# Kernel optimization log

Measured on AMD Instinct MI355X. Metric: run time of the kernel, lower is better.

Reference implementation:

```python
import jax, jax.numpy as jnp
import numpy as np

NSAMPLE = 64
RADIUS = 0.3
HMIN = -0.2
HMAX_LIST = (0.1, 0.2, 0.3, 0.4)
NUM_ANGLE = 12
NUM_DEPTH = 4
EPS = 1e-5


def setup_inputs() -> dict:
    key = jax.random.key(0)
    ks = jax.random.split(key, 32)
    rn = lambda i, s: jax.random.normal(ks[i], s, dtype=jnp.float32)
    ru = lambda i, s: jax.random.uniform(ks[i], s, dtype=jnp.float32)
    return {
        'seed_xyz': rn(0, (2, 1024, 3)),
        'pointcloud': rn(1, (2, 8192, 3)),
        'vp_rot': rn(2, (2, 1024, 3, 3)),
        'cw1': rn(3, (64, 3)), 'cbn1': ru(4, (4, 64)),
        'cw2': rn(5, (128, 64)), 'cbn2': ru(6, (4, 128)),
        'cw3': rn(7, (256, 128)), 'cbn3': ru(8, (4, 256)),
        'ow1': rn(9, (128, 256)), 'ob1': rn(10, (128,)), 'obn1': ru(11, (4, 128)),
        'ow2': rn(12, (128, 128)), 'ob2': rn(13, (128,)), 'obn2': ru(14, (4, 128)),
        'ow3': rn(15, (36, 128)), 'ob3': rn(16, (36,)),
        'tw1': rn(17, (128, 256)), 'tb1': rn(18, (128,)), 'tbn1': ru(19, (4, 128)),
        'tw2': rn(20, (128, 128)), 'tb2': rn(21, (128,)), 'tbn2': ru(22, (4, 128)),
        'tw3': rn(23, (12, 128)), 'tb3': rn(24, (12,)),
    }


def _bn_relu(y, bn):
    g, b, m, v = bn[0], bn[1], bn[2], bn[3]
    return jax.nn.relu(g * (y - m) * jax.lax.rsqrt(v + EPS) + b)


def _bn(y, bn):
    g, b, m, v = bn[0], bn[1], bn[2], bn[3]
    return g * (y - m) * jax.lax.rsqrt(v + EPS) + b


def _forward(seed_xyz, pointcloud, vp_rot, cw1, cbn1, cw2, cbn2, cw3, cbn3,
             ow1, ob1, obn1, ow2, ob2, obn2, ow3, ob3,
             tw1, tb1, tbn1, tw2, tb2, tbn2, tw3, tb3):
    B, ns, _ = seed_xyz.shape
    N = pointcloud.shape[1]
    # relative coords of every scene point w.r.t. every seed, rotated into the
    # grasp-view frame (cylinder axis = x after rotation): (B, ns, N, 3)
    rel = pointcloud[:, None, :, :] - seed_xyz[:, :, None, :]
    rot_rel = jnp.einsum('bsnc,bscd->bsnd', rel, vp_rot)
    ax = rot_rel[..., 0]
    r2 = rot_rel[..., 1] ** 2 + rot_rel[..., 2] ** 2
    pref = jnp.arange(N, dtype=jnp.float32) / N  # earlier index preferred (CUDA scan order)
    groups = []
    for hmax in HMAX_LIST:
        mask = (ax > HMIN) & (ax < hmax) & (r2 < RADIUS * RADIUS)
        score = mask.astype(jnp.float32) * 2.0 - pref
        _, idx = jax.lax.top_k(score, NSAMPLE)  # (B, ns, NSAMPLE), first valid idxs in order
        valid = jnp.take_along_axis(mask, idx, axis=-1)
        idx = jnp.where(valid, idx, idx[..., :1])  # fill slots with first found index
        g = jnp.take_along_axis(rot_rel, idx[..., None], axis=2)  # (B, ns, NSAMPLE, 3)
        groups.append(g)
    feat = jnp.stack(groups, axis=2)  # (B, ns, num_depth, NSAMPLE, 3)
    feat = feat.reshape(B, ns * NUM_DEPTH, NSAMPLE, 3)
    # SharedMLP [3,64,128,256], conv2d 1x1 (no bias) + BN + ReLU
    h = _bn_relu(feat @ cw1.T, cbn1)
    h = _bn_relu(h @ cw2.T, cbn2)
    h = _bn_relu(h @ cw3.T, cbn3)
    vp = jnp.max(h, axis=2)  # max-pool over nsample -> (B, ns*num_depth, 256)

    def head(w1, b1, bn1, w2, b2, bn2, w3, b3):
        x = _bn_relu(vp @ w1.T + b1, bn1)
        x = _bn_relu(x @ w2.T + b2, bn2)
        return x @ w3.T + b3

    op = head(ow1, ob1, obn1, ow2, ob2, obn2, ow3, ob3)     # (B, ns*D, 3*num_angle)
    tol = head(tw1, tb1, tbn1, tw2, tb2, tbn2, tw3, tb3)    # (B, ns*D, num_angle)
    out = jnp.concatenate([op, tol], axis=-1)               # score|angle_cls|width|tolerance
    out = out.reshape(B, ns, NUM_DEPTH, 4 * NUM_ANGLE).transpose(0, 3, 1, 2)
    return out  # (B, 4*num_angle, num_seed, num_depth)


def reference(seed_xyz, pointcloud, vp_rot, cw1, cbn1, cw2, cbn2, cw3, cbn3,
              ow1, ob1, obn1, ow2, ob2, obn2, ow3, ob3,
              tw1, tb1, tbn1, tw2, tb2, tbn2, tw3, tb3):
    return _forward(seed_xyz, pointcloud, vp_rot, cw1, cbn1, cw2, cbn2, cw3, cbn3,
                    ow1, ob1, obn1, ow2, ob2, obn2, ow3, ob3,
                    tw1, tb1, tbn1, tw2, tb2, tbn2, tw3, tb3)
```

## Files before the change

kernel.cpp:

```cpp
#include <hip/hip_runtime.h>
#include <hip/hip_bf16.h>

#define NB    2
#define NS    1024
#define NPTS  8192
#define NGROUP (NB*NS*4)

enum : int {
  OFF_BW2  = 256,
  OFF_W1Q  = 4352,
  OFF_B2   = 8448,
  OFF_BW3  = 8576,
  OFF_B3   = 41344,
  OFF_HB1  = 41600,
  OFF_HB1B = 74368,
  OFF_HB2  = 74624,
  OFF_HB2B = 107392,
  OFF_HB3  = 107648,
  OFF_HB3B = 115840,
  OFF_FEAT = 146688,
  OFF_VP   = 1719552,
  OFF_PCX  = 1719552, OFF_PCY = 1735936, OFF_PCZ = 1752320,
  OFF_SEED = 1768704, OFF_ROT = 1774848,
  OFF_CNT  = 3816704,
  OFF_FLAG = 3824896,
  PREP_TOTAL = 189632 + 6144 + 18432 + 49152,
};

struct Ptrs { const void* p[25]; };

typedef __attribute__((ext_vector_type(8))) short bf16x8;
typedef __attribute__((ext_vector_type(4))) float f32x4;
typedef __attribute__((ext_vector_type(4))) unsigned u32x4;

template<typename T> struct LD;
template<> struct LD<float> {
  static __device__ __forceinline__ float get(const void* p, int i){ return ((const float*)p)[i]; }
};
template<> struct LD<__hip_bfloat16> {
  static __device__ __forceinline__ float get(const void* p, int i){ return __bfloat162float(((const __hip_bfloat16*)p)[i]); }
};

template<typename T>
__device__ __forceinline__ float bnscale(const void* bn, int C, int c){
  float g = LD<T>::get(bn, c);
  float v = LD<T>::get(bn, 3*C + c);
  return g / sqrtf(v + 1e-5f);
}

__device__ __forceinline__ unsigned short f2bf(float v){
  __hip_bfloat16 hb = __float2bfloat16(v);
  return *reinterpret_cast<unsigned short*>(&hb);
}

#if __has_builtin(__builtin_amdgcn_cvt_pk_bf16_f32)
typedef __attribute__((ext_vector_type(2))) __bf16 bf16x2_t;
__device__ __forceinline__ unsigned pk2bf(float a, float b){
  bf16x2_t r = __builtin_amdgcn_cvt_pk_bf16_f32(a, b);
  return *reinterpret_cast<unsigned*>(&r);
}
#else
__device__ __forceinline__ unsigned pk2bf(float a, float b){
  return (unsigned)f2bf(a) | ((unsigned)f2bf(b) << 16);
}
#endif

template<typename T>
__device__ void prep_body(const Ptrs& in, float* __restrict__ ws, int i){
  if (i < 256) { int c = i>>2, d = i&3; float s = bnscale<T>(in.p[4],64,c);
    float v = (d<3) ? LD<T>::get(in.p[3], c*3+d)*s
                    : LD<T>::get(in.p[4],64+c) - LD<T>::get(in.p[4],2*64+c)*s;
    ws[OFF_W1Q+i] = v; return; }
  i -= 256;
  if (i < 8192) {
    int j = i&7, f = i>>3, lane = f&63, kn = f>>6, kt = kn&1, nt = kn>>1;
    int n = nt*16 + (lane&15), k = kt*32 + ((lane>>4)<<3) + j;
    float s = bnscale<T>(in.p[6],128,n);
    ((unsigned short*)(ws + OFF_BW2))[i] = f2bf(LD<T>::get(in.p[5], n*64+k)*s); return; }
  i -= 8192;
  if (i < 32768) {
    int j = i&7, f = i>>3, lane = f&63, kn = f>>6, kt = kn&3, nt = kn>>2;
    int n = nt*16 + (lane&15), k = kt*32 + ((lane>>4)<<3) + j;
    float s = bnscale<T>(in.p[8],256,n);
    ((unsigned short*)(ws + OFF_BW3))[i] = f2bf(LD<T>::get(in.p[7], n*128+k)*s); return; }
  i -= 32768;
  if (i < 128) { float s = bnscale<T>(in.p[6],128,i);
    ws[OFF_B2+i] = LD<T>::get(in.p[6],128+i) - LD<T>::get(in.p[6],2*128+i)*s; return; }
  i -= 128;
  if (i < 256) { float s = bnscale<T>(in.p[8],256,i);
    ws[OFF_B3+i] = LD<T>::get(in.p[8],256+i) - LD<T>::get(in.p[8],2*256+i)*s; return; }
  i -= 256;
  if (i < 65536) {
    int j = i&7, f = i>>3, lane = f&63, kn = f>>6, kt = kn&7, nt = kn>>3;
    int n = nt*16 + (lane&15), k = kt*32 + ((lane>>4)<<3) + j;
    float v;
    if (n < 128) v = LD<T>::get(in.p[9],  n*256+k)       * bnscale<T>(in.p[11],128,n);
    else         v = LD<T>::get(in.p[17], (n-128)*256+k) * bnscale<T>(in.p[19],128,n-128);
    ((unsigned short*)(ws + OFF_HB1))[i] = f2bf(v); return; }
  i -= 65536;
  if (i < 256) { int n = i; float v;
    if (n < 128) { float s = bnscale<T>(in.p[11],128,n);
      v = (LD<T>::get(in.p[10],n) - LD<T>::get(in.p[11],2*128+n))*s + LD<T>::get(in.p[11],128+n); }
    else { int m = n-128; float s = bnscale<T>(in.p[19],128,m);
      v = (LD<T>::get(in.p[18],m) - LD<T>::get(in.p[19],2*128+m))*s + LD<T>::get(in.p[19],128+m); }
    ws[OFF_HB1B+n] = v; return; }
  i -= 256;
  if (i < 65536) {
    int j = i&7, f = i>>3, lane = f&63, kn = f>>6, kt = kn&7, nt = kn>>3;
    int n = nt*16 + (lane&15), k = kt*32 + ((lane>>4)<<3) + j;
    float v = 0.f;
    if (n < 128) { if (k < 128)  v = LD<T>::get(in.p[12], n*128+k)            * bnscale<T>(in.p[14],128,n); }
    else         { if (k >= 128) v = LD<T>::get(in.p[20], (n-128)*128+(k-128)) * bnscale<T>(in.p[22],128,n-128); }
    ((unsigned short*)(ws + OFF_HB2))[i] = f2bf(v); return; }
  i -= 65536;
  if (i < 256) { int n = i; float v;
    if (n < 128) { float s = bnscale<T>(in.p[14],128,n);
      v = (LD<T>::get(in.p[13],n) - LD<T>::get(in.p[14],2*128+n))*s + LD<T>::get(in.p[14],128+n); }
    else { int m = n-128; float s = bnscale<T>(in.p[22],128,m);
      v = (LD<T>::get(in.p[21],m) - LD<T>::get(in.p[22],2*128+m))*s + LD<T>::get(in.p[22],128+m); }
    ws[OFF_HB2B+n] = v; return; }
  i -= 256;
  if (i < 16384) {
    int j = i&7, f = i>>3, lane = f&63, kn = f>>6, kt = kn&7, nt = kn>>3;
    int n = nt*16 + (lane&15), k = kt*32 + ((lane>>4)<<3) + j;
    float v = 0.f;
    if (n < 36)      { if (k < 128)  v = LD<T>::get(in.p[15], n*128+k); }
    else if (n < 48) { if (k >= 128) v = LD<T>::get(in.p[23], (n-36)*128+(k-128)); }
    ((unsigned short*)(ws + OFF_HB3))[i] = f2bf(v); return; }
  i -= 16384;
  if (i < 64) { int n = i; float v = 0.f;
    if (n < 36) v = LD<T>::get(in.p[16], n);
    else if (n < 48) v = LD<T>::get(in.p[24], n-36);
    ws[OFF_HB3B+n] = v; return; }
  i -= 64;
  if (i < 6144)  { ws[OFF_SEED+i] = LD<T>::get(in.p[0], i); return; }
  i -= 6144;
  if (i < 18432) { ws[OFF_ROT+i] = LD<T>::get(in.p[2], i); return; }
  i -= 18432;
  { int arr = i >> 14, idx = i & 16383;
    ws[OFF_PCX + arr*16384 + idx] = LD<T>::get(in.p[1], idx*3 + arr); }
}

__global__ __launch_bounds__(256) void prep_kernel(Ptrs in, float* __restrict__ ws){
  __shared__ int sf;
  const int t = threadIdx.x;
  if (t == 0) sf = 0;
  __syncthreads();
  int loc = 0;
  const uint4* w3r = (const uint4*)in.p[7];
#pragma unroll
  for (int k = 0; k < 2; ++k) {
    uint4 u = w3r[t + k*256];
    loc |= ((u.x & 0x7F80u) == 0x7F80u) | (((u.x>>16) & 0x7F80u) == 0x7F80u);
    loc |= ((u.y & 0x7F80u) == 0x7F80u) | (((u.y>>16) & 0x7F80u) == 0x7F80u);
    loc |= ((u.z & 0x7F80u) == 0x7F80u) | (((u.z>>16) & 0x7F80u) == 0x7F80u);
    loc |= ((u.w & 0x7F80u) == 0x7F80u) | (((u.w>>16) & 0x7F80u) == 0x7F80u);
  }
  if (loc) atomicOr(&sf, 1);
  __syncthreads();
  const int isf32 = sf;
  const int i = blockIdx.x*256 + t;
  if (i == 0) ((int*)(ws + OFF_FLAG))[0] = isf32;
  if (i >= PREP_TOTAL) return;
  if (isf32) prep_body<float>(in, ws, i);
  else       prep_body<__hip_bfloat16>(in, ws, i);
}

__global__ __launch_bounds__(256) void group_kernel(float* __restrict__ ws){
#pragma clang fp contract(off)
  __shared__ float scratch[2][2][4][192];
  __shared__ int   cl[2][2][4];
  __shared__ float p0s[2][3];
  const int t = threadIdx.x;
  const int wave = t >> 6, lane = t & 63;
  const int s = wave >> 1, half = wave & 1;
  const int seedIdx = blockIdx.x*2 + s;
  const int b = seedIdx >> 10;
  const float sx = ws[OFF_SEED + seedIdx*3+0];
  const float sy = ws[OFF_SEED + seedIdx*3+1];
  const float sz = ws[OFF_SEED + seedIdx*3+2];
  const float r00=ws[OFF_ROT+seedIdx*9+0], r01=ws[OFF_ROT+seedIdx*9+1], r02=ws[OFF_ROT+seedIdx*9+2];
  const float r10=ws[OFF_ROT+seedIdx*9+3], r11=ws[OFF_ROT+seedIdx*9+4], r12=ws[OFF_ROT+seedIdx*9+5];
  const float r20=ws[OFF_ROT+seedIdx*9+6], r21=ws[OFF_ROT+seedIdx*9+7], r22=ws[OFF_ROT+seedIdx*9+8];
  const float* px = ws + OFF_PCX + b*8192;
  const float* py = ws + OFF_PCY + b*8192;
  const float* pz = ws + OFF_PCZ + b*8192;
  if (half == 0 && lane == 0) {
    float e0 = px[0] - sx, e1 = py[0] - sy, e2 = pz[0] - sz;
    p0s[s][0] = e0*r00 + e1*r10 + e2*r20;
    p0s[s][1] = e0*r01 + e1*r11 + e2*r21;
    p0s[s][2] = e0*r02 + e1*r12 + e2*r22;
  }
  float* s0 = scratch[s][half][0];
  float* s1 = scratch[s][half][1];
  float* s2 = scratch[s][half][2];
  float* s3 = scratch[s][half][3];
  int c0n=0, c1n=0, c2n=0, c3n=0;
  const int basept = half*4096;
  const unsigned long long pm = (1ull << lane) - 1ull;

  auto scan = [&](float x, float y, float z){
    float e0 = x - sx, e1 = y - sy, e2 = z - sz;
    float rx = e0*r00 + e1*r10 + e2*r20;
    float ry = e0*r01 + e1*r11 + e2*r21;
    float rz = e0*r02 + e1*r12 + e2*r22;
    float r2 = ry*ry + rz*rz;
    const bool mb = (rx > -0.2f) && (r2 < 0.09f);
    const bool l3 = mb && (rx < 0.4f);
    const unsigned long long bal3 = __ballot(l3);
    if (bal3 == 0ull) return;
    { bool m = mb && (rx < 0.1f); unsigned long long bal = __ballot(m);
      if (bal) { int slot = c0n + __popcll(bal & pm);
        if (m && slot < 64) { s0[slot*3]=rx; s0[slot*3+1]=ry; s0[slot*3+2]=rz; }
        c0n += __popcll(bal); } }
    { bool m = mb && (rx < 0.2f); unsigned long long bal = __ballot(m);
      if (bal) { int slot = c1n + __popcll(bal & pm);
        if (m && slot < 64) { s1[slot*3]=rx; s1[slot*3+1]=ry; s1[slot*3+2]=rz; }
        c1n += __popcll(bal); } }
    { bool m = mb && (rx < 0.3f); unsigned long long bal = __ballot(m);
      if (bal) { int slot = c2n + __popcll(bal & pm);
        if (m && slot < 64) { s2[slot*3]=rx; s2[slot*3+1]=ry; s2[slot*3+2]=rz; }
        c2n += __popcll(bal); } }
    { int slot = c3n + __popcll(bal3 & pm);
      if (l3 && slot < 64) { s3[slot*3]=rx; s3[slot*3+1]=ry; s3[slot*3+2]=rz; }
      c3n += __popcll(bal3); }
  };

  for (int c = 0; c < 64; c += 2) {
    const int i0 = basept + c*64 + lane;
    float xA = px[i0],    yA = py[i0],    zA = pz[i0];
    float xB = px[i0+64], yB = py[i0+64], zB = pz[i0+64];
    scan(xA, yA, zA);
    scan(xB, yB, zB);
  }
  if (lane == 0) { cl[s][half][0]=c0n; cl[s][half][1]=c1n; cl[s][half][2]=c2n; cl[s][half][3]=c3n; }
  __syncthreads();
  for (int idx = t; idx < 512; idx += 256) {
    const int ss = idx >> 8, bin = (idx >> 6) & 3, slot = idx & 63;
    int ca = cl[ss][0][bin]; if (ca > 64) ca = 64;
    int cb = cl[ss][1][bin];
    const float* A = scratch[ss][0][bin];
    const float* B = scratch[ss][1][bin];
    float fx, fy, fz;
    if (slot < ca)              { fx=A[slot*3]; fy=A[slot*3+1]; fz=A[slot*3+2]; }
    else if (slot - ca < cb)    { int q = slot-ca; fx=B[q*3]; fy=B[q*3+1]; fz=B[q*3+2]; }
    else if (ca > 0)            { fx=A[0]; fy=A[1]; fz=A[2]; }
    else if (cb > 0)            { fx=B[0]; fy=B[1]; fz=B[2]; }
    else                        { fx=p0s[ss][0]; fy=p0s[ss][1]; fz=p0s[ss][2]; }
    const int g = (blockIdx.x*2 + ss)*4 + bin;
    float* fo = ws + OFF_FEAT + g*192;
    fo[slot*3+0]=fx; fo[slot*3+1]=fy; fo[slot*3+2]=fz;
  }
  if (t < 8) {
    const int ss = t >> 2, bin = t & 3;
    int tot = cl[ss][0][bin] + cl[ss][1][bin];
    if (tot > 64) tot = 64;
    if (tot < 1)  tot = 1;
    const int g = (blockIdx.x*2 + ss)*4 + bin;
    ((int*)(ws + OFF_CNT))[g] = (tot + 15) >> 4;
  }
}

template<int MTS>
__device__ __forceinline__ void mlp_body(float* __restrict__ ws, unsigned short* __restrict__ h2,
                                         const float* __restrict__ wq,
                                         int lane, int quad, int l15, int nhalf, int g){
  const float* feat = ws + OFF_FEAT + g*192;
  float fx[MTS], fy[MTS], fz[MTS];
#pragma unroll
  for (int Nt = 0; Nt < MTS; ++Nt) {
    const int sm = Nt*16 + l15;
    fx[Nt] = feat[sm*3+0]; fy[Nt] = feat[sm*3+1]; fz[Nt] = feat[sm*3+2];
  }
  bf16x8 b1[MTS][2];
#pragma unroll
  for (int kt = 0; kt < 2; ++kt) {
    f32x4 w[8];
#pragma unroll
    for (int j = 0; j < 8; ++j) w[j] = *(const f32x4*)(wq + (kt*32 + quad*8 + j)*4);
#pragma unroll
    for (int Nt = 0; Nt < MTS; ++Nt) {
      const float x0 = fx[Nt], x1 = fy[Nt], x2 = fz[Nt];
      u32x4 p;
#pragma unroll
      for (int jp = 0; jp < 4; ++jp) {
        const f32x4 wa = w[2*jp], wb = w[2*jp+1];
        const float v0 = fmaxf(wa[3] + x0*wa[0] + x1*wa[1] + x2*wa[2], 0.f);
        const float v1 = fmaxf(wb[3] + x0*wb[0] + x1*wb[1] + x2*wb[2], 0.f);
        p[jp] = pk2bf(v0, v1);
      }
      b1[Nt][kt] = __builtin_bit_cast(bf16x8, p);
    }
  }
  const bf16x8* BW2 = (const bf16x8*)(ws + OFF_BW2);
#pragma unroll
  for (int mt4 = 0; mt4 < 4; ++mt4) {
    const int Mt = nhalf*4 + mt4;
    const f32x4 bias4 = *(const f32x4*)(ws + OFF_B2 + Mt*16 + quad*4);
    f32x4 acc[MTS];
#pragma unroll
    for (int Nt = 0; Nt < MTS; ++Nt) acc[Nt] = bias4;
#pragma unroll
    for (int kt = 0; kt < 2; ++kt) {
      const bf16x8 aw = BW2[(Mt*2+kt)*64 + lane];
#pragma unroll
      for (int Nt = 0; Nt < MTS; ++Nt)
        acc[Nt] = __builtin_amdgcn_mfma_f32_16x16x32_bf16(aw, b1[Nt][kt], acc[Nt], 0, 0, 0);
    }
#pragma unroll
    for (int Nt = 0; Nt < MTS; ++Nt) {
      const unsigned lo = pk2bf(fmaxf(acc[Nt][0],0.f), fmaxf(acc[Nt][1],0.f));
      const unsigned hi = pk2bf(fmaxf(acc[Nt][2],0.f), fmaxf(acc[Nt][3],0.f));
      uint2* dst = (uint2*)&h2[(Nt*16 + l15)*136 + Mt*16 + quad*4];
      *dst = make_uint2(lo, hi);
    }
  }
  __syncthreads();
  bf16x8 a2[MTS][4];
#pragma unroll
  for (int mt = 0; mt < MTS; ++mt)
#pragma unroll
    for (int kt = 0; kt < 4; ++kt)
      a2[mt][kt] = *(const bf16x8*)&h2[(mt*16 + l15)*136 + kt*32 + quad*8];
  const bf16x8* BW3 = (const bf16x8*)(ws + OFF_BW3);
  float vpv[8];
#pragma unroll
  for (int nt8 = 0; nt8 < 8; ++nt8) {
    const int nt = nhalf*8 + nt8;
    const int n = nt*16 + l15;
    const float bias = ws[OFF_B3 + n];
    f32x4 acc[MTS];
#pragma unroll
    for (int mt = 0; mt < MTS; ++mt) acc[mt] = (f32x4){bias, bias, bias, bias};
#pragma unroll
    for (int kt = 0; kt < 4; ++kt) {
      const bf16x8 b = BW3[(nt*4+kt)*64 + lane];
#pragma unroll
      for (int mt = 0; mt < MTS; ++mt)
        acc[mt] = __builtin_amdgcn_mfma_f32_16x16x32_bf16(a2[mt][kt], b, acc[mt], 0, 0, 0);
    }
    float mx = 0.f;
#pragma unroll
    for (int mt = 0; mt < MTS; ++mt)
      mx = fmaxf(mx, fmaxf(fmaxf(acc[mt][0], acc[mt][1]), fmaxf(acc[mt][2], acc[mt][3])));
    mx = fmaxf(mx, __shfl_xor(mx, 16, 64));
    mx = fmaxf(mx, __shfl_xor(mx, 32, 64));
    vpv[nt8] = mx;
  }
  if (quad == 0) {
    float* vp = ws + OFF_VP + g*256 + nhalf*128;
#pragma unroll
    for (int nt8 = 0; nt8 < 8; ++nt8) vp[nt8*16 + l15] = vpv[nt8];
  }
}

__global__ __launch_bounds__(256) void mlp_kernel(float* __restrict__ ws){
  __shared__ unsigned short h2s[2][64*136];
  const int blk = blockIdx.x;
  const int g0 = blk*2, g1 = blk*2 + 1;
  const int* cnt = (const int*)(ws + OFF_CNT);
  const int mt0 = cnt[g0], mt1 = cnt[g1];
  const int v = (mt0 > mt1) ? mt0 : mt1;
  const int t = threadIdx.x;
  const int wave = t >> 6, lane = t & 63;
  const int quad = lane >> 4, l15 = lane & 15;
  const int grp = wave >> 1, nhalf = wave & 1;
  const int g = grp ? g1 : g0;
  unsigned short* h2 = h2s[grp];
  const float* wq = ws + OFF_W1Q;
  switch (v) {
    case 1:  mlp_body<1>(ws, h2, wq, lane, quad, l15, nhalf, g); break;
    case 2:  mlp_body<2>(ws, h2, wq, lane, quad, l15, nhalf, g); break;
    case 3:  mlp_body<3>(ws, h2, wq, lane, quad, l15, nhalf, g); break;
    default: mlp_body<4>(ws, h2, wq, lane, quad, l15, nhalf, g); break;
  }
}

#define YSTRIDE 264
__global__ __launch_bounds__(256) void heads_kernel(float* __restrict__ ws, void* __restrict__ outv){
  const int isf32 = ((const volatile int*)(ws + OFF_FLAG))[0];
  __shared__ unsigned short y[16*YSTRIDE];
  const int t = threadIdx.x;
  const int wave = t >> 6, lane = t & 63;
  const int quad = lane >> 4, l15 = lane & 15;
  const int r0 = blockIdx.x * 16;
  bf16x8 a[8];
  const float* vp = ws + OFF_VP + (r0 + l15)*256;
#pragma unroll
  for (int kt = 0; kt < 8; ++kt) {
    const float4* v4 = (const float4*)(vp + kt*32 + quad*8);
    float4 u0 = v4[0], u1 = v4[1];
    a[kt][0]=(short)f2bf(u0.x); a[kt][1]=(short)f2bf(u0.y); a[kt][2]=(short)f2bf(u0.z); a[kt][3]=(short)f2bf(u0.w);
    a[kt][4]=(short)f2bf(u1.x); a[kt][5]=(short)f2bf(u1.y); a[kt][6]=(short)f2bf(u1.z); a[kt][7]=(short)f2bf(u1.w);
  }
  const bf16x8* HB1 = (const bf16x8*)(ws + OFF_HB1);
#pragma unroll
  for (int nt4 = 0; nt4 < 4; ++nt4) {
    const int nt = wave*4 + nt4;
    const int n = nt*16 + l15;
    const float bias = ws[OFF_HB1B + n];
    f32x4 acc = (f32x4){bias, bias, bias, bias};
#pragma unroll
    for (int kt = 0; kt < 8; ++kt)
      acc = __builtin_amdgcn_mfma_f32_16x16x32_bf16(a[kt], HB1[(nt*8+kt)*64 + lane], acc, 0, 0, 0);
#pragma unroll
    for (int jj = 0; jj < 4; ++jj)
      y[(quad*4+jj)*YSTRIDE + n] = f2bf(fmaxf(acc[jj], 0.f));
  }
  __syncthreads();
#pragma unroll
  for (int kt = 0; kt < 8; ++kt)
    a[kt] = *(const bf16x8*)&y[l15*YSTRIDE + kt*32 + quad*8];
  __syncthreads();
  const bf16x8* HB2 = (const bf16x8*)(ws + OFF_HB2);
#pragma unroll
  for (int nt4 = 0; nt4 < 4; ++nt4) {
    const int nt = wave*4 + nt4;
    const int n = nt*16 + l15;
    const float bias = ws[OFF_HB2B + n];
    f32x4 acc = (f32x4){bias, bias, bias, bias};
#pragma unroll
    for (int kt = 0; kt < 8; ++kt)
      acc = __builtin_amdgcn_mfma_f32_16x16x32_bf16(a[kt], HB2[(nt*8+kt)*64 + lane], acc, 0, 0, 0);
#pragma unroll
    for (int jj = 0; jj < 4; ++jj)
      y[(quad*4+jj)*YSTRIDE + n] = f2bf(fmaxf(acc[jj], 0.f));
  }
  __syncthreads();
#pragma unroll
  for (int kt = 0; kt < 8; ++kt)
    a[kt] = *(const bf16x8*)&y[l15*YSTRIDE + kt*32 + quad*8];
  const bf16x8* HB3 = (const bf16x8*)(ws + OFF_HB3);
  {
    const int n = wave*16 + l15;
    const float bias = ws[OFF_HB3B + n];
    f32x4 acc = (f32x4){bias, bias, bias, bias};
#pragma unroll
    for (int kt = 0; kt < 8; ++kt)
      acc = __builtin_amdgcn_mfma_f32_16x16x32_bf16(a[kt], HB3[(wave*8+kt)*64 + lane], acc, 0, 0, 0);
    if (n < 48) {
#pragma unroll
      for (int jj = 0; jj < 4; ++jj) {
        const int gr = r0 + quad*4 + jj;
        const int b = gr >> 12, rem = gr & 4095, s = rem >> 2, d = rem & 3;
        const int o = ((b*48 + n)*1024 + s)*4 + d;
        if (isf32) ((float*)outv)[o] = acc[jj];
        else       ((__hip_bfloat16*)outv)[o] = __float2bfloat16(acc[jj]);
      }
    }
  }
}

extern "C" void kernel_launch(void* const* d_in, const int* in_sizes, int n_in,
                              void* d_out, int out_size, void* d_ws, size_t ws_size,
                              hipStream_t stream) {
  float* ws = (float*)d_ws;
  Ptrs P;
  for (int i = 0; i < 25; ++i) P.p[i] = d_in[i];
  prep_kernel<<<(PREP_TOTAL+255)/256, 256, 0, stream>>>(P, ws);
  group_kernel<<<NB*NS/2, 256, 0, stream>>>(ws);
  mlp_kernel<<<NGROUP/2, 256, 0, stream>>>(ws);
  heads_kernel<<<NGROUP/16, 256, 0, stream>>>(ws, d_out);
}
```

Measured before the change: 206.3 us.

## Fuse grouping, shared MLP and heads into one kernel using LDS intermediates

Result: no change. 208.0 us (+0.8%).

```diff
diff --git a/kernel.cpp b/kernel.cpp
--- a/kernel.cpp
+++ b/kernel.cpp
@@ -18,11 +18,8 @@
   OFF_HB2B = 107392,
   OFF_HB3  = 107648,
   OFF_HB3B = 115840,
-  OFF_FEAT = 146688,
-  OFF_VP   = 1719552,
   OFF_PCX  = 1719552, OFF_PCY = 1735936, OFF_PCZ = 1752320,
   OFF_SEED = 1768704, OFF_ROT = 1774848,
-  OFF_CNT  = 3816704,
   OFF_FLAG = 3824896,
   PREP_TOTAL = 189632 + 6144 + 18432 + 49152,
 };
@@ -166,15 +163,14 @@
   else       prep_body<__hip_bfloat16>(in, ws, i);
 }
 
-__global__ __launch_bounds__(256) void group_kernel(float* __restrict__ ws){
+__device__ void group_phase(const float* __restrict__ ws, float* __restrict__ scratch,
+                            int* __restrict__ cl, float* __restrict__ p0s,
+                            float* __restrict__ featL, int* __restrict__ mtL,
+                            int blk, int t){
 #pragma clang fp contract(off)
-  __shared__ float scratch[2][2][4][192];
-  __shared__ int   cl[2][2][4];
-  __shared__ float p0s[2][3];
-  const int t = threadIdx.x;
   const int wave = t >> 6, lane = t & 63;
   const int s = wave >> 1, half = wave & 1;
-  const int seedIdx = blockIdx.x*2 + s;
+  const int seedIdx = blk*2 + s;
   const int b = seedIdx >> 10;
   const float sx = ws[OFF_SEED + seedIdx*3+0];
   const float sy = ws[OFF_SEED + seedIdx*3+1];
@@ -187,14 +183,14 @@
   const float* pz = ws + OFF_PCZ + b*8192;
   if (half == 0 && lane == 0) {
     float e0 = px[0] - sx, e1 = py[0] - sy, e2 = pz[0] - sz;
-    p0s[s][0] = e0*r00 + e1*r10 + e2*r20;
-    p0s[s][1] = e0*r01 + e1*r11 + e2*r21;
-    p0s[s][2] = e0*r02 + e1*r12 + e2*r22;
-  }
-  float* s0 = scratch[s][half][0];
-  float* s1 = scratch[s][half][1];
-  float* s2 = scratch[s][half][2];
-  float* s3 = scratch[s][half][3];
+    p0s[s*3+0] = e0*r00 + e1*r10 + e2*r20;
+    p0s[s*3+1] = e0*r01 + e1*r11 + e2*r21;
+    p0s[s*3+2] = e0*r02 + e1*r12 + e2*r22;
+  }
+  float* s0 = scratch + ((s*2+half)*4+0)*192;
+  float* s1 = scratch + ((s*2+half)*4+1)*192;
+  float* s2 = scratch + ((s*2+half)*4+2)*192;
+  float* s3 = scratch + ((s*2+half)*4+3)*192;
   int c0n=0, c1n=0, c2n=0, c3n=0;
   const int basept = half*4096;
   const unsigned long long pm = (1ull << lane) - 1ull;
@@ -233,44 +229,45 @@
     scan(xA, yA, zA);
     scan(xB, yB, zB);
   }
-  if (lane == 0) { cl[s][half][0]=c0n; cl[s][half][1]=c1n; cl[s][half][2]=c2n; cl[s][half][3]=c3n; }
+  if (lane == 0) {
+    cl[(s*2+half)*4+0]=c0n; cl[(s*2+half)*4+1]=c1n;
+    cl[(s*2+half)*4+2]=c2n; cl[(s*2+half)*4+3]=c3n;
+  }
   __syncthreads();
   for (int idx = t; idx < 512; idx += 256) {
     const int ss = idx >> 8, bin = (idx >> 6) & 3, slot = idx & 63;
-    int ca = cl[ss][0][bin]; if (ca > 64) ca = 64;
-    int cb = cl[ss][1][bin];
-    const float* A = scratch[ss][0][bin];
-    const float* B = scratch[ss][1][bin];
+    int ca = cl[(ss*2+0)*4+bin]; if (ca > 64) ca = 64;
+    int cb = cl[(ss*2+1)*4+bin];
+    const float* A = scratch + ((ss*2+0)*4+bin)*192;
+    const float* B = scratch + ((ss*2+1)*4+bin)*192;
     float fx, fy, fz;
     if (slot < ca)              { fx=A[slot*3]; fy=A[slot*3+1]; fz=A[slot*3+2]; }
     else if (slot - ca < cb)    { int q = slot-ca; fx=B[q*3]; fy=B[q*3+1]; fz=B[q*3+2]; }
     else if (ca > 0)            { fx=A[0]; fy=A[1]; fz=A[2]; }
     else if (cb > 0)            { fx=B[0]; fy=B[1]; fz=B[2]; }
-    else                        { fx=p0s[ss][0]; fy=p0s[ss][1]; fz=p0s[ss][2]; }
-    const int g = (blockIdx.x*2 + ss)*4 + bin;
-    float* fo = ws + OFF_FEAT + g*192;
+    else                        { fx=p0s[ss*3+0]; fy=p0s[ss*3+1]; fz=p0s[ss*3+2]; }
+    float* fo = featL + (ss*4+bin)*192;
     fo[slot*3+0]=fx; fo[slot*3+1]=fy; fo[slot*3+2]=fz;
   }
   if (t < 8) {
     const int ss = t >> 2, bin = t & 3;
-    int tot = cl[ss][0][bin] + cl[ss][1][bin];
+    int tot = cl[(ss*2+0)*4+bin] + cl[(ss*2+1)*4+bin];
     if (tot > 64) tot = 64;
     if (tot < 1)  tot = 1;
-    const int g = (blockIdx.x*2 + ss)*4 + bin;
-    ((int*)(ws + OFF_CNT))[g] = (tot + 15) >> 4;
+    mtL[t] = (tot + 15) >> 4;
   }
 }
 
 template<int MTS>
-__device__ __forceinline__ void mlp_body(float* __restrict__ ws, unsigned short* __restrict__ h2,
-                                         const float* __restrict__ wq,
-                                         int lane, int quad, int l15, int nhalf, int g){
-  const float* feat = ws + OFF_FEAT + g*192;
+__device__ __forceinline__ void mlp_body(const float* __restrict__ ws, unsigned short* __restrict__ h2,
+                                         const float* __restrict__ wq, const float* __restrict__ featp,
+                                         float* __restrict__ vpp,
+                                         int lane, int quad, int l15, int nhalf){
   float fx[MTS], fy[MTS], fz[MTS];
 #pragma unroll
   for (int Nt = 0; Nt < MTS; ++Nt) {
     const int sm = Nt*16 + l15;
-    fx[Nt] = feat[sm*3+0]; fy[Nt] = feat[sm*3+1]; fz[Nt] = feat[sm*3+2];
+    fx[Nt] = featp[sm*3+0]; fy[Nt] = featp[sm*3+1]; fz[Nt] = featp[sm*3+2];
   }
   bf16x8 b1[MTS][2];
 #pragma unroll
@@ -348,104 +345,120 @@
     vpv[nt8] = mx;
   }
   if (quad == 0) {
-    float* vp = ws + OFF_VP + g*256 + nhalf*128;
-#pragma unroll
-    for (int nt8 = 0; nt8 < 8; ++nt8) vp[nt8*16 + l15] = vpv[nt8];
-  }
-}
-
-__global__ __launch_bounds__(256) void mlp_kernel(float* __restrict__ ws){
-  __shared__ unsigned short h2s[2][64*136];
-  const int blk = blockIdx.x;
-  const int g0 = blk*2, g1 = blk*2 + 1;
-  const int* cnt = (const int*)(ws + OFF_CNT);
-  const int mt0 = cnt[g0], mt1 = cnt[g1];
-  const int v = (mt0 > mt1) ? mt0 : mt1;
+#pragma unroll
+    for (int nt8 = 0; nt8 < 8; ++nt8) vpp[nhalf*128 + nt8*16 + l15] = vpv[nt8];
+  }
+}
+
+#define YSTRIDE 264
+__global__ __launch_bounds__(256) void fused_kernel(float* __restrict__ ws, void* __restrict__ outv){
+  __shared__ __align__(16) char ubuf[34816];
+  __shared__ float featL[8*192];
+  __shared__ float vpL[8*256];
+  __shared__ int   mtL[8];
+  __shared__ float w1qL[1024];
   const int t = threadIdx.x;
   const int wave = t >> 6, lane = t & 63;
   const int quad = lane >> 4, l15 = lane & 15;
-  const int grp = wave >> 1, nhalf = wave & 1;
-  const int g = grp ? g1 : g0;
-  unsigned short* h2 = h2s[grp];
-  const float* wq = ws + OFF_W1Q;
-  switch (v) {
-    case 1:  mlp_body<1>(ws, h2, wq, lane, quad, l15, nhalf, g); break;
-    case 2:  mlp_body<2>(ws, h2, wq, lane, quad, l15, nhalf, g); break;
-    case 3:  mlp_body<3>(ws, h2, wq, lane, quad, l15, nhalf, g); break;
-    default: mlp_body<4>(ws, h2, wq, lane, quad, l15, nhalf, g); break;
-  }
-}
-
-#define YSTRIDE 264
-__global__ __launch_bounds__(256) void heads_kernel(float* __restrict__ ws, void* __restrict__ outv){
-  const int isf32 = ((const volatile int*)(ws + OFF_FLAG))[0];
-  __shared__ unsigned short y[16*YSTRIDE];
-  const int t = threadIdx.x;
-  const int wave = t >> 6, lane = t & 63;
-  const int quad = lane >> 4, l15 = lane & 15;
-  const int r0 = blockIdx.x * 16;
-  bf16x8 a[8];
-  const float* vp = ws + OFF_VP + (r0 + l15)*256;
-#pragma unroll
-  for (int kt = 0; kt < 8; ++kt) {
-    const float4* v4 = (const float4*)(vp + kt*32 + quad*8);
-    float4 u0 = v4[0], u1 = v4[1];
-    a[kt][0]=(short)f2bf(u0.x); a[kt][1]=(short)f2bf(u0.y); a[kt][2]=(short)f2bf(u0.z); a[kt][3]=(short)f2bf(u0.w);
-    a[kt][4]=(short)f2bf(u1.x); a[kt][5]=(short)f2bf(u1.y); a[kt][6]=(short)f2bf(u1.z); a[kt][7]=(short)f2bf(u1.w);
-  }
-  const bf16x8* HB1 = (const bf16x8*)(ws + OFF_HB1);
-#pragma unroll
-  for (int nt4 = 0; nt4 < 4; ++nt4) {
-    const int nt = wave*4 + nt4;
-    const int n = nt*16 + l15;
-    const float bias = ws[OFF_HB1B + n];
-    f32x4 acc = (f32x4){bias, bias, bias, bias};
+  const int blk = blockIdx.x;
+
+  for (int i = t; i < 1024; i += 256) w1qL[i] = ws[OFF_W1Q + i];
+
+  group_phase(ws, (float*)ubuf, (int*)(ubuf + 12288), (float*)(ubuf + 12288 + 64),
+              featL, mtL, blk, t);
+  __syncthreads();
+
+  {
+    const int grp = wave >> 1, nhalf = wave & 1;
+    unsigned short* h2 = (unsigned short*)ubuf + grp*(64*136);
+    for (int pair = 0; pair < 4; ++pair) {
+      const int m0 = mtL[pair*2], m1 = mtL[pair*2+1];
+      const int v = (m0 > m1) ? m0 : m1;
+      const int lg = pair*2 + grp;
+      const float* featp = featL + lg*192;
+      float* vpp = vpL + lg*256;
+      switch (v) {
+        case 1:  mlp_body<1>(ws, h2, w1qL, featp, vpp, lane, quad, l15, nhalf); break;
+        case 2:  mlp_body<2>(ws, h2, w1qL, featp, vpp, lane, quad, l15, nhalf); break;
+        case 3:  mlp_body<3>(ws, h2, w1qL, featp, vpp, lane, quad, l15, nhalf); break;
+        default: mlp_body<4>(ws, h2, w1qL, featp, vpp, lane, quad, l15, nhalf); break;
+      }
+      __syncthreads();
+    }
+  }
+
+  {
+    const int isf32 = ((const volatile int*)(ws + OFF_FLAG))[0];
+    unsigned short* y = (unsigned short*)ubuf;
+    bf16x8 a[8];
+    if (l15 < 8) {
+      const float* vp = vpL + l15*256;
+#pragma unroll
+      for (int kt = 0; kt < 8; ++kt) {
+        const float4* v4 = (const float4*)(vp + kt*32 + quad*8);
+        float4 u0 = v4[0], u1 = v4[1];
+        a[kt][0]=(short)f2bf(u0.x); a[kt][1]=(short)f2bf(u0.y); a[kt][2]=(short)f2bf(u0.z); a[kt][3]=(short)f2bf(u0.w);
+        a[kt][4]=(short)f2bf(u1.x); a[kt][5]=(short)f2bf(u1.y); a[kt][6]=(short)f2bf(u1.z); a[kt][7]=(short)f2bf(u1.w);
+      }
+    } else {
+      const u32x4 z = (u32x4){0,0,0,0};
+#pragma unroll
+      for (int kt = 0; kt < 8; ++kt) a[kt] = __builtin_bit_cast(bf16x8, z);
+    }
+    const bf16x8* HB1 = (const bf16x8*)(ws + OFF_HB1);
+#pragma unroll
+    for (int nt4 = 0; nt4 < 4; ++nt4) {
+      const int nt = wave*4 + nt4;
+      const int n = nt*16 + l15;
+      const float bias = ws[OFF_HB1B + n];
+      f32x4 acc = (f32x4){bias, bias, bias, bias};
+#pragma unroll
+      for (int kt = 0; kt < 8; ++kt)
+        acc = __builtin_amdgcn_mfma_f32_16x16x32_bf16(a[kt], HB1[(nt*8+kt)*64 + lane], acc, 0, 0, 0);
+#pragma unroll
+      for (int jj = 0; jj < 4; ++jj)
+        y[(quad*4+jj)*YSTRIDE + n] = f2bf(fmaxf(acc[jj], 0.f));
+    }
+    __syncthreads();
 #pragma unroll
     for (int kt = 0; kt < 8; ++kt)
-      acc = __builtin_amdgcn_mfma_f32_16x16x32_bf16(a[kt], HB1[(nt*8+kt)*64 + lane], acc, 0, 0, 0);
-#pragma unroll
-    for (int jj = 0; jj < 4; ++jj)
-      y[(quad*4+jj)*YSTRIDE + n] = f2bf(fmaxf(acc[jj], 0.f));
-  }
-  __syncthreads();
-#pragma unroll
-  for (int kt = 0; kt < 8; ++kt)
-    a[kt] = *(const bf16x8*)&y[l15*YSTRIDE + kt*32 + quad*8];
-  __syncthreads();
-  const bf16x8* HB2 = (const bf16x8*)(ws + OFF_HB2);
-#pragma unroll
-  for (int nt4 = 0; nt4 < 4; ++nt4) {
-    const int nt = wave*4 + nt4;
-    const int n = nt*16 + l15;
-    const float bias = ws[OFF_HB2B + n];
-    f32x4 acc = (f32x4){bias, bias, bias, bias};
+      a[kt] = *(const bf16x8*)&y[l15*YSTRIDE + kt*32 + quad*8];
+    __syncthreads();
+    const bf16x8* HB2 = (const bf16x8*)(ws + OFF_HB2);
+#pragma unroll
+    for (int nt4 = 0; nt4 < 4; ++nt4) {
+      const int nt = wave*4 + nt4;
+      const int n = nt*16 + l15;
+      const float bias = ws[OFF_HB2B + n];
+      f32x4 acc = (f32x4){bias, bias, bias, bias};
+#pragma unroll
+      for (int kt = 0; kt < 8; ++kt)
+        acc = __builtin_amdgcn_mfma_f32_16x16x32_bf16(a[kt], HB2[(nt*8+kt)*64 + lane], acc, 0, 0, 0);
+#pragma unroll
+      for (int jj = 0; jj < 4; ++jj)
+        y[(quad*4+jj)*YSTRIDE + n] = f2bf(fmaxf(acc[jj], 0.f));
+    }
+    __syncthreads();
 #pragma unroll
     for (int kt = 0; kt < 8; ++kt)
-      acc = __builtin_amdgcn_mfma_f32_16x16x32_bf16(a[kt], HB2[(nt*8+kt)*64 + lane], acc, 0, 0, 0);
-#pragma unroll
-    for (int jj = 0; jj < 4; ++jj)
-      y[(quad*4+jj)*YSTRIDE + n] = f2bf(fmaxf(acc[jj], 0.f));
-  }
-  __syncthreads();
-#pragma unroll
-  for (int kt = 0; kt < 8; ++kt)
-    a[kt] = *(const bf16x8*)&y[l15*YSTRIDE + kt*32 + quad*8];
-  const bf16x8* HB3 = (const bf16x8*)(ws + OFF_HB3);
-  {
-    const int n = wave*16 + l15;
-    const float bias = ws[OFF_HB3B + n];
-    f32x4 acc = (f32x4){bias, bias, bias, bias};
-#pragma unroll
-    for (int kt = 0; kt < 8; ++kt)
-      acc = __builtin_amdgcn_mfma_f32_16x16x32_bf16(a[kt], HB3[(wave*8+kt)*64 + lane], acc, 0, 0, 0);
-    if (n < 48) {
-#pragma unroll
-      for (int jj = 0; jj < 4; ++jj) {
-        const int gr = r0 + quad*4 + jj;
-        const int b = gr >> 12, rem = gr & 4095, s = rem >> 2, d = rem & 3;
-        const int o = ((b*48 + n)*1024 + s)*4 + d;
-        if (isf32) ((float*)outv)[o] = acc[jj];
-        else       ((__hip_bfloat16*)outv)[o] = __float2bfloat16(acc[jj]);
+      a[kt] = *(const bf16x8*)&y[l15*YSTRIDE + kt*32 + quad*8];
+    const bf16x8* HB3 = (const bf16x8*)(ws + OFF_HB3);
+    {
+      const int n = wave*16 + l15;
+      const float bias = ws[OFF_HB3B + n];
+      f32x4 acc = (f32x4){bias, bias, bias, bias};
+#pragma unroll
+      for (int kt = 0; kt < 8; ++kt)
+        acc = __builtin_amdgcn_mfma_f32_16x16x32_bf16(a[kt], HB3[(wave*8+kt)*64 + lane], acc, 0, 0, 0);
+      if (n < 48 && quad < 2) {
+#pragma unroll
+        for (int jj = 0; jj < 4; ++jj) {
+          const int gr = blk*8 + quad*4 + jj;
+          const int b = gr >> 12, rem = gr & 4095, s = rem >> 2, d = rem & 3;
+          const int o = ((b*48 + n)*1024 + s)*4 + d;
+          if (isf32) ((float*)outv)[o] = acc[jj];
+          else       ((__hip_bfloat16*)outv)[o] = __float2bfloat16(acc[jj]);
+        }
       }
     }
   }
@@ -458,7 +471,5 @@
   Ptrs P;
   for (int i = 0; i < 25; ++i) P.p[i] = d_in[i];
   prep_kernel<<<(PREP_TOTAL+255)/256, 256, 0, stream>>>(P, ws);
-  group_kernel<<<NB*NS/2, 256, 0, stream>>>(ws);
-  mlp_kernel<<<NGROUP/2, 256, 0, stream>>>(ws);
-  heads_kernel<<<NGROUP/16, 256, 0, stream>>>(ws, d_out);
-}
+  fused_kernel<<<NB*NS/2, 256, 0, stream>>>(ws, d_out);
+}
```
